# Performance work log

Hardware: AMD Instinct MI355X
Metric: run time of the kernel (lower is better)

Reference implementation:

```python
import jax, jax.numpy as jnp
import numpy as np

N_NODES = 100000
N_EDGES = 1600000
D_IN = 128
D_HID = 64
BN_EPS = 1e-5


def setup_inputs() -> dict:
    key = jax.random.key(0)
    ks = jax.random.split(key, 8)
    x = jax.random.normal(ks[0], (N_NODES, D_IN), dtype=jnp.float32)
    edge_index = jax.random.randint(ks[1], (2, N_EDGES), 0, N_NODES, dtype=jnp.int64)
    # GCNConv1 weight/bias (glorot-ish scale)
    W1 = jax.random.normal(ks[2], (D_IN, D_HID), dtype=jnp.float32) / np.sqrt(D_IN)
    b1 = jnp.zeros((D_HID,), dtype=jnp.float32)
    # BatchNorm1d (eval mode: running stats)
    gamma = jax.random.normal(ks[3], (D_HID,), dtype=jnp.float32) * 0.1 + 1.0
    beta = jax.random.normal(ks[4], (D_HID,), dtype=jnp.float32) * 0.1
    run_mean = jnp.zeros((D_HID,), dtype=jnp.float32)
    run_var = jnp.ones((D_HID,), dtype=jnp.float32)
    # fc1: Linear(2*hidden, 2)
    Wfc = jax.random.normal(ks[5], (2 * D_HID, 2), dtype=jnp.float32) / np.sqrt(2 * D_HID)
    bfc = jnp.zeros((2,), dtype=jnp.float32)
    return {"x": x, "edge_index": edge_index, "W1": W1, "b1": b1,
            "gamma": gamma, "beta": beta, "run_mean": run_mean, "run_var": run_var,
            "Wfc": Wfc, "bfc": bfc}


def gcn_conv(x, edge_index, W, b):
    # PyG GCNConv: add self-loops, symmetric normalization, scatter-add aggregation
    n = x.shape[0]
    loops = jnp.arange(n, dtype=edge_index.dtype)
    row = jnp.concatenate([edge_index[0], loops])  # source nodes
    col = jnp.concatenate([edge_index[1], loops])  # target nodes
    deg = jax.ops.segment_sum(jnp.ones_like(col, dtype=x.dtype), col, num_segments=n)
    dinv = jax.lax.rsqrt(jnp.maximum(deg, 1.0))  # deg >= 1 due to self-loops
    norm = dinv[row] * dinv[col]                 # [E+N]
    h = x @ W                                    # [N, hid]
    msgs = h[row] * norm[:, None]                # gather + scale  [E+N, hid]
    out = jax.ops.segment_sum(msgs, col, num_segments=n)  # scatter-add
    return out + b


def reference(x, edge_index, W1, b1, gamma, beta, run_mean, run_var, Wfc, bfc):
    h = gcn_conv(x, edge_index, W1, b1)
    h = jax.nn.relu(h)
    # dropout(p=0.9) is identity in eval mode
    # BatchNorm1d eval: normalize with running stats
    h = (h - run_mean) * jax.lax.rsqrt(run_var + BN_EPS) * gamma + beta
    h = jax.nn.relu(h)
    # edge gather-concat-linear
    er = jnp.concatenate([h[edge_index[0]], h[edge_index[1]]], axis=1)  # [E, 2*hid]
    return er @ Wfc + bfc  # [E, 2]
```

## Files before the change

kernel.cpp:

```cpp
#include <hip/hip_runtime.h>

#define N_NODES 100000
#define N_EDGES 1600000
#define D_IN 128
#define D_HID 64
#define BN_EPS 1e-5f

#define BUCKET_SHIFT 7
#define BUCKET_W 128
#define N_BUCKETS ((N_NODES + BUCKET_W - 1) / BUCKET_W)
#define BCAP 4096
#define N_BIN_BLOCKS 256
#define EDGES_PER_BLOCK (N_EDGES / N_BIN_BLOCKS)
#define GT 2

typedef __attribute__((ext_vector_type(8))) short bf16x8;
typedef __attribute__((ext_vector_type(4))) float f32x4;
typedef __attribute__((ext_vector_type(8))) _Float16 f16x8;

__device__ __forceinline__ ushort f2bf(float f) {
    unsigned u = __float_as_uint(f);
    u += 0x7FFF + ((u >> 16) & 1);
    return (ushort)(u >> 16);
}

__global__ __launch_bounds__(256) void bin_scatter_kernel(const int* __restrict__ row,
                                                          const int* __restrict__ col,
                                                          int* __restrict__ bcursor,
                                                          int* __restrict__ binned) {
    __shared__ int hist[N_BUCKETS];
    __shared__ int lbase[N_BUCKETS];
    const int t = threadIdx.x;
    for (int i = t; i < N_BUCKETS; i += 256) hist[i] = 0;
    __syncthreads();
    const int e0 = blockIdx.x * EDGES_PER_BLOCK;
    for (int j = t; j < EDGES_PER_BLOCK; j += 256)
        atomicAdd(&hist[col[e0 + j] >> BUCKET_SHIFT], 1);
    __syncthreads();
    for (int i = t; i < N_BUCKETS; i += 256) {
        int h = hist[i];
        lbase[i] = h ? (i * BCAP + atomicAdd(&bcursor[i], h)) : 0;
        hist[i] = 0;
    }
    __syncthreads();
    for (int j = t; j < EDGES_PER_BLOCK; j += 256) {
        int c = col[e0 + j];
        int r = row[e0 + j];
        int b = c >> BUCKET_SHIFT;
        int rank = atomicAdd(&hist[b], 1);
        binned[lbase[b] + rank] = ((c & (BUCKET_W - 1)) << 17) | r;
    }
}

__global__ __launch_bounds__(256) void bucket_csr_kernel(const int* __restrict__ binned,
                                                         const int* __restrict__ bcursor,
                                                         int* __restrict__ csr_src,
                                                         int2* __restrict__ rs2,
                                                         float* __restrict__ dinv) {
    __shared__ int hist[BUCKET_W];
    __shared__ int cursor[BUCKET_W];
    const int b = blockIdx.x;
    const int t = threadIdx.x;
    if (t < BUCKET_W) hist[t] = 0;
    __syncthreads();
    const int s = b * BCAP;
    const int e = s + bcursor[b];
    for (int i = s + t; i < e; i += 256)
        atomicAdd(&hist[binned[i] >> 17], 1);
    __syncthreads();
    if (t < BUCKET_W) cursor[t] = hist[t];
    for (int off = 1; off < BUCKET_W; off <<= 1) {
        __syncthreads();
        int add = (t >= off && t < BUCKET_W) ? cursor[t - off] : 0;
        __syncthreads();
        if (t < BUCKET_W) cursor[t] += add;
    }
    __syncthreads();
    int excl = (t < BUCKET_W) ? (cursor[t] - hist[t]) : 0;
    __syncthreads();
    if (t < BUCKET_W) cursor[t] = excl;
    const int node = b * BUCKET_W + t;
    if (t < BUCKET_W && node < N_NODES) {
        rs2[node] = make_int2(s + excl, hist[t]);
        dinv[node] = rsqrtf(1.0f + (float)hist[t]);
    }
    __syncthreads();
    for (int i = s + t; i < e; i += 256) {
        int p = binned[i];
        int pos = atomicAdd(&cursor[p >> 17], 1);
        csr_src[s + pos] = p & 0x1FFFF;
    }
}

__global__ __launch_bounds__(256) void gemm_mfma_kernel(const float* __restrict__ x,
                                                        const float* __restrict__ W,
                                                        const float* __restrict__ dinv,
                                                        ushort* __restrict__ h_s) {
    __shared__ ushort xb[16 * 136];
    const int t = threadIdx.x;
    const int l = t & 63;
    const int wv = t >> 6;
    const int q = l >> 4;
    const int m = l & 15;
    bf16x8 bf[4];
    {
        const int n = wv * 16 + m;
        #pragma unroll
        for (int s = 0; s < 4; ++s)
            #pragma unroll
            for (int j = 0; j < 8; ++j)
                bf[s][j] = (short)f2bf(W[(32 * s + 8 * q + j) * D_HID + n]);
    }
    for (int tile = 0; tile < GT; ++tile) {
        const int node0 = blockIdx.x * (16 * GT) + tile * 16;
        __syncthreads();
        for (int i = t; i < 512; i += 256) {
            int r = i >> 5, c4 = i & 31;
            float4 v = *(const float4*)&x[(size_t)(node0 + r) * D_IN + c4 * 4];
            ushort4 u = make_ushort4(f2bf(v.x), f2bf(v.y), f2bf(v.z), f2bf(v.w));
            *(ushort4*)&xb[r * 136 + c4 * 4] = u;
        }
        __syncthreads();
        f32x4 acc = {0.f, 0.f, 0.f, 0.f};
        #pragma unroll
        for (int s = 0; s < 4; ++s) {
            bf16x8 af = *(const bf16x8*)&xb[m * 136 + 32 * s + 8 * q];
            acc = __builtin_amdgcn_mfma_f32_16x16x32_bf16(af, bf[s], acc, 0, 0, 0);
        }
        #pragma unroll
        for (int r = 0; r < 4; ++r) {
            int node = node0 + q * 4 + r;
            _Float16 hv = (_Float16)(acc[r] * dinv[node]);
            h_s[node * D_HID + wv * 16 + m] = __builtin_bit_cast(unsigned short, hv);
        }
    }
}

__global__ __launch_bounds__(256) void aggregate_kernel(const ushort* __restrict__ h_s,
                                                        const float* __restrict__ dinv,
                                                        const int2* __restrict__ rs2,
                                                        const int* __restrict__ csr_src,
                                                        const float* __restrict__ b1,
                                                        const float* __restrict__ gamma,
                                                        const float* __restrict__ beta,
                                                        const float* __restrict__ mean,
                                                        const float* __restrict__ var,
                                                        const float* __restrict__ Wfc,
                                                        float4* __restrict__ uv) {
    const f16x8* __restrict__ hsv = (const f16x8*)h_s;
    const int wvid = (blockIdx.x * 256 + threadIdx.x) >> 6;
    const int lane = threadIdx.x & 63;
    const int oct = lane >> 3;
    const int ol = lane & 7;
    const int n = wvid * 8 + oct;
    f16x8 acc = hsv[n * 8 + ol];
    const int2 rs = rs2[n];
    const int start = rs.x;
    const int cnt = rs.y;
    int j = 0;
    for (; j + 8 <= cnt; j += 8) {
        int i0 = csr_src[start + j + 0];
        int i1 = csr_src[start + j + 1];
        int i2 = csr_src[start + j + 2];
        int i3 = csr_src[start + j + 3];
        int i4 = csr_src[start + j + 4];
        int i5 = csr_src[start + j + 5];
        int i6 = csr_src[start + j + 6];
        int i7 = csr_src[start + j + 7];
        f16x8 v0 = hsv[i0 * 8 + ol];
        f16x8 v1 = hsv[i1 * 8 + ol];
        f16x8 v2 = hsv[i2 * 8 + ol];
        f16x8 v3 = hsv[i3 * 8 + ol];
        f16x8 v4 = hsv[i4 * 8 + ol];
        f16x8 v5 = hsv[i5 * 8 + ol];
        f16x8 v6 = hsv[i6 * 8 + ol];
        f16x8 v7 = hsv[i7 * 8 + ol];
        acc += v0; acc += v1; acc += v2; acc += v3;
        acc += v4; acc += v5; acc += v6; acc += v7;
    }
    for (; j + 4 <= cnt; j += 4) {
        int i0 = csr_src[start + j + 0];
        int i1 = csr_src[start + j + 1];
        int i2 = csr_src[start + j + 2];
        int i3 = csr_src[start + j + 3];
        f16x8 v0 = hsv[i0 * 8 + ol];
        f16x8 v1 = hsv[i1 * 8 + ol];
        f16x8 v2 = hsv[i2 * 8 + ol];
        f16x8 v3 = hsv[i3 * 8 + ol];
        acc += v0; acc += v1; acc += v2; acc += v3;
    }
    for (; j + 2 <= cnt; j += 2) {
        int i0 = csr_src[start + j + 0];
        int i1 = csr_src[start + j + 1];
        f16x8 v0 = hsv[i0 * 8 + ol];
        f16x8 v1 = hsv[i1 * 8 + ol];
        acc += v0; acc += v1;
    }
    if (j < cnt)
        acc += hsv[csr_src[start + j] * 8 + ol];
    const float dn = dinv[n];
    const int f0 = 8 * ol;
    float a[8];
    #pragma unroll
    for (int k = 0; k < 8; ++k) a[k] = (float)acc[k] * dn;
    float bb[8], mu[8], vr[8], gm[8], bt[8];
    *(float4*)&bb[0] = *(const float4*)&b1[f0];    *(float4*)&bb[4] = *(const float4*)&b1[f0 + 4];
    *(float4*)&mu[0] = *(const float4*)&mean[f0];  *(float4*)&mu[4] = *(const float4*)&mean[f0 + 4];
    *(float4*)&vr[0] = *(const float4*)&var[f0];   *(float4*)&vr[4] = *(const float4*)&var[f0 + 4];
    *(float4*)&gm[0] = *(const float4*)&gamma[f0]; *(float4*)&gm[4] = *(const float4*)&gamma[f0 + 4];
    *(float4*)&bt[0] = *(const float4*)&beta[f0];  *(float4*)&bt[4] = *(const float4*)&beta[f0 + 4];
    #pragma unroll
    for (int k = 0; k < 8; ++k) {
        float v = fmaxf(a[k] + bb[k], 0.f);
        a[k] = fmaxf((v - mu[k]) * rsqrtf(vr[k] + BN_EPS) * gm[k] + bt[k], 0.f);
    }
    float wt[16], wb[16];
    #pragma unroll
    for (int k = 0; k < 4; ++k) {
        *(float4*)&wt[4 * k] = *(const float4*)&Wfc[2 * f0 + 4 * k];
        *(float4*)&wb[4 * k] = *(const float4*)&Wfc[128 + 2 * f0 + 4 * k];
    }
    float p0 = 0.f, p1 = 0.f, p2 = 0.f, p3 = 0.f;
    #pragma unroll
    for (int k = 0; k < 8; ++k) {
        p0 += a[k] * wt[2 * k];
        p1 += a[k] * wt[2 * k + 1];
        p2 += a[k] * wb[2 * k];
        p3 += a[k] * wb[2 * k + 1];
    }
    #pragma unroll
    for (int off = 4; off > 0; off >>= 1) {
        p0 += __shfl_xor(p0, off, 64);
        p1 += __shfl_xor(p1, off, 64);
        p2 += __shfl_xor(p2, off, 64);
        p3 += __shfl_xor(p3, off, 64);
    }
    if (ol == 0) uv[n] = make_float4(p0, p1, p2, p3);
}

__global__ __launch_bounds__(256) void edgeout_kernel(const int* __restrict__ row,
                                                      const int* __restrict__ col,
                                                      const float4* __restrict__ uv,
                                                      const float* __restrict__ bfc,
                                                      float2* __restrict__ out) {
    int i = blockIdx.x * 256 + threadIdx.x;
    int e = i * 2;
    int2 rr = *(const int2*)&row[e];
    int2 cc = *(const int2*)&col[e];
    float4 a0 = uv[rr.x];
    float4 b0 = uv[cc.x];
    float4 a1 = uv[rr.y];
    float4 b1 = uv[cc.y];
    float c0 = bfc[0], c1 = bfc[1];
    float4 o = make_float4(a0.x + b0.z + c0, a0.y + b0.w + c1,
                           a1.x + b1.z + c0, a1.y + b1.w + c1);
    *(float4*)&out[e] = o;
}

extern "C" void kernel_launch(void* const* d_in, const int* in_sizes, int n_in,
                              void* d_out, int out_size, void* d_ws, size_t ws_size,
                              hipStream_t stream) {
    const float* x     = (const float*)d_in[0];
    const int*   ei    = (const int*)d_in[1];
    const int*   row   = ei;
    const int*   col   = ei + N_EDGES;
    const float* W1    = (const float*)d_in[2];
    const float* b1    = (const float*)d_in[3];
    const float* gamma = (const float*)d_in[4];
    const float* beta  = (const float*)d_in[5];
    const float* mean  = (const float*)d_in[6];
    const float* var   = (const float*)d_in[7];
    const float* Wfc   = (const float*)d_in[8];
    const float* bfc   = (const float*)d_in[9];
    float2* out = (float2*)d_out;

    char* ws = (char*)d_ws;
    size_t off = 0;
    ushort* h_s      = (ushort*)(ws + off); off += (size_t)N_NODES * D_HID * 2;
    int*   binned    = (int*)(ws + off);    off += (size_t)N_BUCKETS * BCAP * 4;
    int*   csr_src   = (int*)(ws + off);    off += (size_t)N_BUCKETS * BCAP * 4;
    int*   bcursor   = (int*)(ws + off);    off += ((size_t)N_BUCKETS * 4 + 15) & ~(size_t)15;
    int2*  rs2       = (int2*)(ws + off);   off += (size_t)N_NODES * 8;
    float* dinv      = (float*)(ws + off);  off += (size_t)N_NODES * 4;
    float4* uv       = (float4*)(ws + off); off += (size_t)N_NODES * 16;

    hipMemsetAsync(bcursor, 0, N_BUCKETS * sizeof(int), stream);
    bin_scatter_kernel<<<N_BIN_BLOCKS, 256, 0, stream>>>(row, col, bcursor, binned);
    bucket_csr_kernel<<<N_BUCKETS, 256, 0, stream>>>(binned, bcursor, csr_src, rs2, dinv);
    gemm_mfma_kernel<<<N_NODES / (16 * GT), 256, 0, stream>>>(x, W1, dinv, h_s);
    aggregate_kernel<<<N_NODES / 32, 256, 0, stream>>>(h_s, dinv, rs2, csr_src,
                                                       b1, gamma, beta, mean, var,
                                                       Wfc, uv);
    edgeout_kernel<<<N_EDGES / 512, 256, 0, stream>>>(row, col, uv, bfc, out);
}
```

Measured before the change: 203.7 us.

## Fuse bucket CSR build into aggregation via shared memory and global degree atomics

Removes the separate bucket_csr kernel. The per-bucket counting sort now happens in shared memory inside the aggregate kernel, which uses one 512-thread block per 128-node bucket. Node degrees are counted with global atomics in the binning kernel, so the GEMM computes dinv directly. This saves a launch and the global CSR write and read, at the cost of 1.6M global atomics, lower aggregation parallelism (one block per bucket), and an ECAP=2560 shared-memory cap on edges per bucket.

```diff
diff --git a/kernel.cpp b/kernel.cpp
--- a/kernel.cpp
+++ b/kernel.cpp
@@ -10,6 +10,7 @@
 #define BUCKET_W 128
 #define N_BUCKETS ((N_NODES + BUCKET_W - 1) / BUCKET_W)
 #define BCAP 4096
+#define ECAP 2560
 #define N_BIN_BLOCKS 256
 #define EDGES_PER_BLOCK (N_EDGES / N_BIN_BLOCKS)
 #define GT 2
@@ -26,6 +27,7 @@
 
 __global__ __launch_bounds__(256) void bin_scatter_kernel(const int* __restrict__ row,
                                                           const int* __restrict__ col,
+                                                          int* __restrict__ deg,
                                                           int* __restrict__ bcursor,
                                                           int* __restrict__ binned) {
     __shared__ int hist[N_BUCKETS];
@@ -34,8 +36,11 @@
     for (int i = t; i < N_BUCKETS; i += 256) hist[i] = 0;
     __syncthreads();
     const int e0 = blockIdx.x * EDGES_PER_BLOCK;
-    for (int j = t; j < EDGES_PER_BLOCK; j += 256)
-        atomicAdd(&hist[col[e0 + j] >> BUCKET_SHIFT], 1);
+    for (int j = t; j < EDGES_PER_BLOCK; j += 256) {
+        int c = col[e0 + j];
+        atomicAdd(&hist[c >> BUCKET_SHIFT], 1);
+        atomicAdd(&deg[c], 1);
+    }
     __syncthreads();
     for (int i = t; i < N_BUCKETS; i += 256) {
         int h = hist[i];
@@ -52,49 +57,9 @@
     }
 }
 
-__global__ __launch_bounds__(256) void bucket_csr_kernel(const int* __restrict__ binned,
-                                                         const int* __restrict__ bcursor,
-                                                         int* __restrict__ csr_src,
-                                                         int2* __restrict__ rs2,
-                                                         float* __restrict__ dinv) {
-    __shared__ int hist[BUCKET_W];
-    __shared__ int cursor[BUCKET_W];
-    const int b = blockIdx.x;
-    const int t = threadIdx.x;
-    if (t < BUCKET_W) hist[t] = 0;
-    __syncthreads();
-    const int s = b * BCAP;
-    const int e = s + bcursor[b];
-    for (int i = s + t; i < e; i += 256)
-        atomicAdd(&hist[binned[i] >> 17], 1);
-    __syncthreads();
-    if (t < BUCKET_W) cursor[t] = hist[t];
-    for (int off = 1; off < BUCKET_W; off <<= 1) {
-        __syncthreads();
-        int add = (t >= off && t < BUCKET_W) ? cursor[t - off] : 0;
-        __syncthreads();
-        if (t < BUCKET_W) cursor[t] += add;
-    }
-    __syncthreads();
-    int excl = (t < BUCKET_W) ? (cursor[t] - hist[t]) : 0;
-    __syncthreads();
-    if (t < BUCKET_W) cursor[t] = excl;
-    const int node = b * BUCKET_W + t;
-    if (t < BUCKET_W && node < N_NODES) {
-        rs2[node] = make_int2(s + excl, hist[t]);
-        dinv[node] = rsqrtf(1.0f + (float)hist[t]);
-    }
-    __syncthreads();
-    for (int i = s + t; i < e; i += 256) {
-        int p = binned[i];
-        int pos = atomicAdd(&cursor[p >> 17], 1);
-        csr_src[s + pos] = p & 0x1FFFF;
-    }
-}
-
 __global__ __launch_bounds__(256) void gemm_mfma_kernel(const float* __restrict__ x,
                                                         const float* __restrict__ W,
-                                                        const float* __restrict__ dinv,
+                                                        const int* __restrict__ deg,
                                                         ushort* __restrict__ h_s) {
     __shared__ ushort xb[16 * 136];
     const int t = threadIdx.x;
@@ -130,16 +95,16 @@
         #pragma unroll
         for (int r = 0; r < 4; ++r) {
             int node = node0 + q * 4 + r;
-            _Float16 hv = (_Float16)(acc[r] * dinv[node]);
+            float dn = rsqrtf(1.0f + (float)deg[node]);
+            _Float16 hv = (_Float16)(acc[r] * dn);
             h_s[node * D_HID + wv * 16 + m] = __builtin_bit_cast(unsigned short, hv);
         }
     }
 }
 
-__global__ __launch_bounds__(256) void aggregate_kernel(const ushort* __restrict__ h_s,
-                                                        const float* __restrict__ dinv,
-                                                        const int2* __restrict__ rs2,
-                                                        const int* __restrict__ csr_src,
+__global__ __launch_bounds__(512) void aggregate_kernel(const ushort* __restrict__ h_s,
+                                                        const int* __restrict__ bcursor,
+                                                        const int* __restrict__ binned,
                                                         const float* __restrict__ b1,
                                                         const float* __restrict__ gamma,
                                                         const float* __restrict__ beta,
@@ -147,95 +112,132 @@
                                                         const float* __restrict__ var,
                                                         const float* __restrict__ Wfc,
                                                         float4* __restrict__ uv) {
+    __shared__ int eb[ECAP];
+    __shared__ int csr[ECAP];
+    __shared__ int hist[BUCKET_W];
+    __shared__ int cursor[BUCKET_W];
+    __shared__ int startsh[BUCKET_W];
+    const int b = blockIdx.x;
+    const int t = threadIdx.x;
+    if (t < BUCKET_W) hist[t] = 0;
+    __syncthreads();
+    const int s = b * BCAP;
+    const int cnt = bcursor[b];
+    for (int i = t; i < cnt; i += 512) {
+        int p = binned[s + i];
+        eb[i] = p;
+        atomicAdd(&hist[p >> 17], 1);
+    }
+    __syncthreads();
+    if (t < BUCKET_W) cursor[t] = hist[t];
+    for (int off = 1; off < BUCKET_W; off <<= 1) {
+        __syncthreads();
+        int add = (t >= off && t < BUCKET_W) ? cursor[t - off] : 0;
+        __syncthreads();
+        if (t < BUCKET_W) cursor[t] += add;
+    }
+    __syncthreads();
+    if (t < BUCKET_W) {
+        int excl = cursor[t] - hist[t];
+        startsh[t] = excl;
+        cursor[t] = excl;
+    }
+    __syncthreads();
+    for (int i = t; i < cnt; i += 512) {
+        int p = eb[i];
+        int pos = atomicAdd(&cursor[p >> 17], 1);
+        csr[pos] = p & 0x1FFFF;
+    }
+    __syncthreads();
     const f16x8* __restrict__ hsv = (const f16x8*)h_s;
-    const int wvid = (blockIdx.x * 256 + threadIdx.x) >> 6;
-    const int lane = threadIdx.x & 63;
-    const int oct = lane >> 3;
-    const int ol = lane & 7;
-    const int n = wvid * 8 + oct;
-    f16x8 acc = hsv[n * 8 + ol];
-    const int2 rs = rs2[n];
-    const int start = rs.x;
-    const int cnt = rs.y;
-    int j = 0;
-    for (; j + 8 <= cnt; j += 8) {
-        int i0 = csr_src[start + j + 0];
-        int i1 = csr_src[start + j + 1];
-        int i2 = csr_src[start + j + 2];
-        int i3 = csr_src[start + j + 3];
-        int i4 = csr_src[start + j + 4];
-        int i5 = csr_src[start + j + 5];
-        int i6 = csr_src[start + j + 6];
-        int i7 = csr_src[start + j + 7];
-        f16x8 v0 = hsv[i0 * 8 + ol];
-        f16x8 v1 = hsv[i1 * 8 + ol];
-        f16x8 v2 = hsv[i2 * 8 + ol];
-        f16x8 v3 = hsv[i3 * 8 + ol];
-        f16x8 v4 = hsv[i4 * 8 + ol];
-        f16x8 v5 = hsv[i5 * 8 + ol];
-        f16x8 v6 = hsv[i6 * 8 + ol];
-        f16x8 v7 = hsv[i7 * 8 + ol];
-        acc += v0; acc += v1; acc += v2; acc += v3;
-        acc += v4; acc += v5; acc += v6; acc += v7;
-    }
-    for (; j + 4 <= cnt; j += 4) {
-        int i0 = csr_src[start + j + 0];
-        int i1 = csr_src[start + j + 1];
-        int i2 = csr_src[start + j + 2];
-        int i3 = csr_src[start + j + 3];
-        f16x8 v0 = hsv[i0 * 8 + ol];
-        f16x8 v1 = hsv[i1 * 8 + ol];
-        f16x8 v2 = hsv[i2 * 8 + ol];
-        f16x8 v3 = hsv[i3 * 8 + ol];
-        acc += v0; acc += v1; acc += v2; acc += v3;
-    }
-    for (; j + 2 <= cnt; j += 2) {
-        int i0 = csr_src[start + j + 0];
-        int i1 = csr_src[start + j + 1];
-        f16x8 v0 = hsv[i0 * 8 + ol];
-        f16x8 v1 = hsv[i1 * 8 + ol];
-        acc += v0; acc += v1;
-    }
-    if (j < cnt)
-        acc += hsv[csr_src[start + j] * 8 + ol];
-    const float dn = dinv[n];
-    const int f0 = 8 * ol;
-    float a[8];
+    const int ol = t & 7;
     #pragma unroll
-    for (int k = 0; k < 8; ++k) a[k] = (float)acc[k] * dn;
-    float bb[8], mu[8], vr[8], gm[8], bt[8];
-    *(float4*)&bb[0] = *(const float4*)&b1[f0];    *(float4*)&bb[4] = *(const float4*)&b1[f0 + 4];
-    *(float4*)&mu[0] = *(const float4*)&mean[f0];  *(float4*)&mu[4] = *(const float4*)&mean[f0 + 4];
-    *(float4*)&vr[0] = *(const float4*)&var[f0];   *(float4*)&vr[4] = *(const float4*)&var[f0 + 4];
-    *(float4*)&gm[0] = *(const float4*)&gamma[f0]; *(float4*)&gm[4] = *(const float4*)&gamma[f0 + 4];
-    *(float4*)&bt[0] = *(const float4*)&beta[f0];  *(float4*)&bt[4] = *(const float4*)&beta[f0 + 4];
-    #pragma unroll
-    for (int k = 0; k < 8; ++k) {
-        float v = fmaxf(a[k] + bb[k], 0.f);
-        a[k] = fmaxf((v - mu[k]) * rsqrtf(vr[k] + BN_EPS) * gm[k] + bt[k], 0.f);
-    }
-    float wt[16], wb[16];
-    #pragma unroll
-    for (int k = 0; k < 4; ++k) {
-        *(float4*)&wt[4 * k] = *(const float4*)&Wfc[2 * f0 + 4 * k];
-        *(float4*)&wb[4 * k] = *(const float4*)&Wfc[128 + 2 * f0 + 4 * k];
-    }
-    float p0 = 0.f, p1 = 0.f, p2 = 0.f, p3 = 0.f;
-    #pragma unroll
-    for (int k = 0; k < 8; ++k) {
-        p0 += a[k] * wt[2 * k];
-        p1 += a[k] * wt[2 * k + 1];
-        p2 += a[k] * wb[2 * k];
-        p3 += a[k] * wb[2 * k + 1];
-    }
-    #pragma unroll
-    for (int off = 4; off > 0; off >>= 1) {
-        p0 += __shfl_xor(p0, off, 64);
-        p1 += __shfl_xor(p1, off, 64);
-        p2 += __shfl_xor(p2, off, 64);
-        p3 += __shfl_xor(p3, off, 64);
-    }
-    if (ol == 0) uv[n] = make_float4(p0, p1, p2, p3);
+    for (int r = 0; r < 2; ++r) {
+        const int nl = (t >> 3) + r * 64;
+        const int node = b * BUCKET_W + nl;
+        f16x8 acc = hsv[node * 8 + ol];
+        const int st = startsh[nl];
+        const int cn = hist[nl];
+        int j = 0;
+        for (; j + 8 <= cn; j += 8) {
+            int i0 = csr[st + j + 0];
+            int i1 = csr[st + j + 1];
+            int i2 = csr[st + j + 2];
+            int i3 = csr[st + j + 3];
+            int i4 = csr[st + j + 4];
+            int i5 = csr[st + j + 5];
+            int i6 = csr[st + j + 6];
+            int i7 = csr[st + j + 7];
+            f16x8 v0 = hsv[i0 * 8 + ol];
+            f16x8 v1 = hsv[i1 * 8 + ol];
+            f16x8 v2 = hsv[i2 * 8 + ol];
+            f16x8 v3 = hsv[i3 * 8 + ol];
+            f16x8 v4 = hsv[i4 * 8 + ol];
+            f16x8 v5 = hsv[i5 * 8 + ol];
+            f16x8 v6 = hsv[i6 * 8 + ol];
+            f16x8 v7 = hsv[i7 * 8 + ol];
+            acc += v0; acc += v1; acc += v2; acc += v3;
+            acc += v4; acc += v5; acc += v6; acc += v7;
+        }
+        for (; j + 4 <= cn; j += 4) {
+            int i0 = csr[st + j + 0];
+            int i1 = csr[st + j + 1];
+            int i2 = csr[st + j + 2];
+            int i3 = csr[st + j + 3];
+            f16x8 v0 = hsv[i0 * 8 + ol];
+            f16x8 v1 = hsv[i1 * 8 + ol];
+            f16x8 v2 = hsv[i2 * 8 + ol];
+            f16x8 v3 = hsv[i3 * 8 + ol];
+            acc += v0; acc += v1; acc += v2; acc += v3;
+        }
+        for (; j + 2 <= cn; j += 2) {
+            int i0 = csr[st + j + 0];
+            int i1 = csr[st + j + 1];
+            f16x8 v0 = hsv[i0 * 8 + ol];
+            f16x8 v1 = hsv[i1 * 8 + ol];
+            acc += v0; acc += v1;
+        }
+        if (j < cn)
+            acc += hsv[csr[st + j] * 8 + ol];
+        const float dn = rsqrtf(1.0f + (float)cn);
+        const int f0 = 8 * ol;
+        float a[8];
+        #pragma unroll
+        for (int k = 0; k < 8; ++k) a[k] = (float)acc[k] * dn;
+        float bb[8], mu[8], vr[8], gm[8], bt[8];
+        *(float4*)&bb[0] = *(const float4*)&b1[f0];    *(float4*)&bb[4] = *(const float4*)&b1[f0 + 4];
+        *(float4*)&mu[0] = *(const float4*)&mean[f0];  *(float4*)&mu[4] = *(const float4*)&mean[f0 + 4];
+        *(float4*)&vr[0] = *(const float4*)&var[f0];   *(float4*)&vr[4] = *(const float4*)&var[f0 + 4];
+        *(float4*)&gm[0] = *(const float4*)&gamma[f0]; *(float4*)&gm[4] = *(const float4*)&gamma[f0 + 4];
+        *(float4*)&bt[0] = *(const float4*)&beta[f0];  *(float4*)&bt[4] = *(const float4*)&beta[f0 + 4];
+        #pragma unroll
+        for (int k = 0; k < 8; ++k) {
+            float v = fmaxf(a[k] + bb[k], 0.f);
+            a[k] = fmaxf((v - mu[k]) * rsqrtf(vr[k] + BN_EPS) * gm[k] + bt[k], 0.f);
+        }
+        float wt[16], wb[16];
+        #pragma unroll
+        for (int k = 0; k < 4; ++k) {
+            *(float4*)&wt[4 * k] = *(const float4*)&Wfc[2 * f0 + 4 * k];
+            *(float4*)&wb[4 * k] = *(const float4*)&Wfc[128 + 2 * f0 + 4 * k];
+        }
+        float p0 = 0.f, p1 = 0.f, p2 = 0.f, p3 = 0.f;
+        #pragma unroll
+        for (int k = 0; k < 8; ++k) {
+            p0 += a[k] * wt[2 * k];
+            p1 += a[k] * wt[2 * k + 1];
+            p2 += a[k] * wb[2 * k];
+            p3 += a[k] * wb[2 * k + 1];
+        }
+        #pragma unroll
+        for (int off = 4; off > 0; off >>= 1) {
+            p0 += __shfl_xor(p0, off, 64);
+            p1 += __shfl_xor(p1, off, 64);
+            p2 += __shfl_xor(p2, off, 64);
+            p3 += __shfl_xor(p3, off, 64);
+        }
+        if (ol == 0 && node < N_NODES) uv[node] = make_float4(p0, p1, p2, p3);
+    }
 }
 
 __global__ __launch_bounds__(256) void edgeout_kernel(const int* __restrict__ row,
@@ -278,18 +280,15 @@
     size_t off = 0;
     ushort* h_s      = (ushort*)(ws + off); off += (size_t)N_NODES * D_HID * 2;
     int*   binned    = (int*)(ws + off);    off += (size_t)N_BUCKETS * BCAP * 4;
-    int*   csr_src   = (int*)(ws + off);    off += (size_t)N_BUCKETS * BCAP * 4;
+    int*   deg       = (int*)(ws + off);    off += (size_t)N_NODES * 4;
     int*   bcursor   = (int*)(ws + off);    off += ((size_t)N_BUCKETS * 4 + 15) & ~(size_t)15;
-    int2*  rs2       = (int2*)(ws + off);   off += (size_t)N_NODES * 8;
-    float* dinv      = (float*)(ws + off);  off += (size_t)N_NODES * 4;
     float4* uv       = (float4*)(ws + off); off += (size_t)N_NODES * 16;
 
-    hipMemsetAsync(bcursor, 0, N_BUCKETS * sizeof(int), stream);
-    bin_scatter_kernel<<<N_BIN_BLOCKS, 256, 0, stream>>>(row, col, bcursor, binned);
-    bucket_csr_kernel<<<N_BUCKETS, 256, 0, stream>>>(binned, bcursor, csr_src, rs2, dinv);
-    gemm_mfma_kernel<<<N_NODES / (16 * GT), 256, 0, stream>>>(x, W1, dinv, h_s);
-    aggregate_kernel<<<N_NODES / 32, 256, 0, stream>>>(h_s, dinv, rs2, csr_src,
-                                                       b1, gamma, beta, mean, var,
-                                                       Wfc, uv);
+    hipMemsetAsync(deg, 0, (size_t)(N_NODES + N_BUCKETS) * sizeof(int) + 16, stream);
+    bin_scatter_kernel<<<N_BIN_BLOCKS, 256, 0, stream>>>(row, col, deg, bcursor, binned);
+    gemm_mfma_kernel<<<N_NODES / (16 * GT), 256, 0, stream>>>(x, W1, deg, h_s);
+    aggregate_kernel<<<N_BUCKETS, 512, 0, stream>>>(h_s, bcursor, binned,
+                                                    b1, gamma, beta, mean, var,
+                                                    Wfc, uv);
     edgeout_kernel<<<N_EDGES / 512, 256, 0, stream>>>(row, col, uv, bfc, out);
 }
```

After: 251.8 us. 23.6% more time.
